# Performance work log

Hardware: AMD Instinct MI355X
Metric: run time of the kernel (lower is better)

The kernel has to match this reference:

```python
import jax, jax.numpy as jnp
import numpy as np

B, S, H, E = 8, 4096, 1024, 8
TEMPERATURE = 1.0


def setup_inputs() -> dict:
    key = jax.random.key(0)
    ks = jax.random.split(key, 7)
    s_h = 1.0 / np.sqrt(H).astype(np.float32)
    s_h2 = 1.0 / np.sqrt(H // 2).astype(np.float32)
    return {
        "hidden_states": jax.random.normal(ks[0], (B, S, H), jnp.float32),
        # routing_network: Linear(H, H//2) -> ReLU -> Linear(H//2, E)
        "W1": jax.random.normal(ks[1], (H, H // 2), jnp.float32) * s_h,
        "b1": jnp.zeros((H // 2,), jnp.float32),
        "W2": jax.random.normal(ks[2], (H // 2, E), jnp.float32) * s_h2,
        "b2": jnp.zeros((E,), jnp.float32),
        # per-expert dense transform (fixed stand-in for torch.randn-per-call)
        "expert_W": jax.random.normal(ks[3], (E, H, H), jnp.float32) * s_h,
        "expert_b": jax.random.normal(ks[4], (E, H), jnp.float32),
    }


def reference(hidden_states, W1, b1, W2, b2, expert_W, expert_b):
    # Routing network -> logits [B, S, E]
    h = jax.nn.relu(jnp.einsum("bsh,hf->bsf", hidden_states, W1) + b1)
    logits = jnp.einsum("bsf,fe->bse", h, W2) + b2
    probs = jax.nn.softmax(logits / TEMPERATURE, axis=-1)
    # top-1 expert per token (scores are NOT applied to output in the original)
    sel = jnp.argmax(probs, axis=-1)  # [B, S] int
    out = jnp.zeros_like(hidden_states)
    for e in range(E):  # small fixed loop over experts
        mask = (sel == e)[..., None].astype(hidden_states.dtype)  # [B, S, 1]
        xe = hidden_states * mask
        ye = jnp.einsum("bsh,hd->bsd", xe, expert_W[e]) + expert_b[e]
        out = out + ye * mask
    return out
```

## Files before the change

kernel.cpp:

```cpp
#include <hip/hip_runtime.h>
#include <hip/hip_bf16.h>
#include <stdint.h>

#define NTOK 32768
#define HD 1024
#define FD 512
#define NEXP 8
#define TAU 0.05f
#define TAU2 4e-4f

typedef __attribute__((ext_vector_type(8))) short short8;
typedef __attribute__((ext_vector_type(4))) float f32x4;

__device__ __forceinline__ short f2bh(float f) {
  uint32_t u = __float_as_uint(f);
  return (short)((u + 0x7fffu + ((u >> 16) & 1u)) >> 16);
}
__device__ __forceinline__ float bh2f(short h) {
  return __uint_as_float(((uint32_t)(uint16_t)h) << 16);
}

__device__ __forceinline__ void gl16(void* lds, const void* g) {
  __builtin_amdgcn_global_load_lds(
      (const __attribute__((address_space(1))) void*)g,
      (__attribute__((address_space(3))) void*)lds, 16, 0, 0);
}

#define WAITBAR(N)                                              \
  do {                                                          \
    asm volatile("s_waitcnt vmcnt(" #N ")" ::: "memory");       \
    __builtin_amdgcn_s_barrier();                               \
    asm volatile("" ::: "memory");                              \
  } while (0)
#define BARO()                                                  \
  do {                                                          \
    asm volatile("" ::: "memory");                              \
    __builtin_amdgcn_s_barrier();                               \
    asm volatile("" ::: "memory");                              \
  } while (0)

__global__ __launch_bounds__(256) void k_convert(const float* __restrict__ x,
                                                 short* __restrict__ xbf) {
  size_t i = ((size_t)blockIdx.x * 256 + threadIdx.x) * 8;
  f32x4 v0 = *(const f32x4*)(x + i);
  f32x4 v1 = *(const f32x4*)(x + i + 4);
  short8 o;
#pragma unroll
  for (int q = 0; q < 4; ++q) { o[q] = f2bh(v0[q]); o[4 + q] = f2bh(v1[q]); }
  *(short8*)(xbf + i) = o;
}

__global__ __launch_bounds__(256) void k_transpose(
    const float* __restrict__ src, short* __restrict__ dst, int rows, int cols) {
  __shared__ float tile[32][33];
  size_t msz = (size_t)rows * cols;
  src += (size_t)blockIdx.z * msz;
  dst += (size_t)blockIdx.z * msz;
  int c0 = blockIdx.x * 32, r0 = blockIdx.y * 32;
  int tx = threadIdx.x & 31, ty = threadIdx.x >> 5;
#pragma unroll
  for (int i = 0; i < 32; i += 8)
    tile[ty + i][tx] = src[(size_t)(r0 + ty + i) * cols + c0 + tx];
  __syncthreads();
#pragma unroll
  for (int i = 0; i < 32; i += 8)
    dst[(size_t)(c0 + ty + i) * rows + r0 + tx] = f2bh(tile[tx][ty + i]);
}

__global__ __launch_bounds__(256) void k_transpose_split(
    const float* __restrict__ src, short* __restrict__ dstH,
    short* __restrict__ dstL, int rows, int cols) {
  __shared__ float tile[32][33];
  int c0 = blockIdx.x * 32, r0 = blockIdx.y * 32;
  int tx = threadIdx.x & 31, ty = threadIdx.x >> 5;
#pragma unroll
  for (int i = 0; i < 32; i += 8)
    tile[ty + i][tx] = src[(size_t)(r0 + ty + i) * cols + c0 + tx];
  __syncthreads();
#pragma unroll
  for (int i = 0; i < 32; i += 8) {
    float v = tile[tx][ty + i];
    short h = f2bh(v);
    size_t di = (size_t)(c0 + ty + i) * rows + r0 + tx;
    dstH[di] = h;
    dstL[di] = f2bh(v - bh2f(h));
  }
}

template <bool ABF>
__global__ __launch_bounds__(256) void k_gemm1(
    const short* __restrict__ xbf, const float* __restrict__ xf,
    const short* __restrict__ W1T, const float* __restrict__ b1,
    const float* __restrict__ W2, float* __restrict__ part) {
  __shared__ __align__(16) char smem[39168];

  const int tid = threadIdx.x;
  const int lane = tid & 63, wave = tid >> 6;
  const int wr = wave >> 1, wc = wave & 1;
  const int fr = lane & 15, fg = lane >> 4;
  const int bx = ((blockIdx.x & 7) << 5) | (blockIdx.x >> 3);
  const int m0 = bx * 128, n0 = blockIdx.y * 128;
  const int by = blockIdx.y;

  const int r0 = wave * 16 + (lane >> 2);
  const int lsw = (((lane & 3) ^ ((lane >> 3) & 3)) << 3);
  const short* b0p = W1T + (size_t)(n0 + r0) * HD + lsw;
  const short* b1p = W1T + (size_t)(n0 + r0 + 64) * HD + lsw;

  const short* a0p = nullptr; const short* a1p = nullptr;
  const float* aF = nullptr;
  int ar = 0, ah = 0, p0e = 0, p1e = 0;
  if constexpr (ABF) {
    a0p = xbf + (size_t)(m0 + r0) * HD + lsw;
    a1p = xbf + (size_t)(m0 + r0 + 64) * HD + lsw;
  } else {
    ar = tid >> 1; ah = tid & 1;
    aF = xf + (size_t)(m0 + ar) * HD + ah * 16;
    int s = (ar >> 1) & 3;
    p0e = ((2 * ah) ^ s) << 3;
    p1e = p0e ^ 8;
  }

  f32x4 acc[4][4];
#pragma unroll
  for (int i = 0; i < 4; ++i)
#pragma unroll
    for (int j = 0; j < 4; ++j) acc[i][j] = (f32x4){0.f, 0.f, 0.f, 0.f};

  auto STAGE = [&](int kt, int b) {
    const int k0 = kt * 32;
    gl16(smem + 16384 + b * 8192 + wave * 1024, b0p + k0);
    gl16(smem + 16384 + b * 8192 + 4096 + wave * 1024, b1p + k0);
    if constexpr (ABF) {
      gl16(smem + b * 8192 + wave * 1024, a0p + k0);
      gl16(smem + b * 8192 + 4096 + wave * 1024, a1p + k0);
    } else {
      f32x4 u0 = *(const f32x4*)(aF + k0);
      f32x4 u1 = *(const f32x4*)(aF + k0 + 4);
      f32x4 u2 = *(const f32x4*)(aF + k0 + 8);
      f32x4 u3 = *(const f32x4*)(aF + k0 + 12);
      short8 s0, s1;
#pragma unroll
      for (int q = 0; q < 4; ++q) {
        s0[q] = f2bh(u0[q]); s0[4 + q] = f2bh(u1[q]);
        s1[q] = f2bh(u2[q]); s1[4 + q] = f2bh(u3[q]);
      }
      short* As = (short*)(smem + b * 8192);
      *(short8*)(As + ar * 32 + p0e) = s0;
      *(short8*)(As + ar * 32 + p1e) = s1;
    }
  };
  const int csw = (fr >> 1) & 3;
  auto COMPUTE = [&](int b) {
    const short* As = (const short*)(smem + b * 8192);
    const short* Bs = (const short*)(smem + 16384 + b * 8192);
    short8 af[4], bf4[4];
#pragma unroll
    for (int i = 0; i < 4; ++i) {
      af[i]  = *(const short8*)(As + (wr * 64 + i * 16 + fr) * 32 + ((fg ^ csw) << 3));
      bf4[i] = *(const short8*)(Bs + (wc * 64 + i * 16 + fr) * 32 + ((fg ^ csw) << 3));
    }
#pragma unroll
    for (int i = 0; i < 4; ++i)
#pragma unroll
      for (int j = 0; j < 4; ++j)
        acc[i][j] = __builtin_amdgcn_mfma_f32_16x16x32_bf16(af[i], bf4[j], acc[i][j], 0, 0, 0);
  };

  STAGE(0, 0);
  if constexpr (ABF) WAITBAR(0); else __syncthreads();
#pragma unroll 1
  for (int kt = 0; kt < 32; kt += 2) {
    STAGE(kt + 1, 1);
    if constexpr (ABF) WAITBAR(4); else __syncthreads();
    COMPUTE(0);
    if constexpr (ABF) BARO(); else __syncthreads();
    if (kt + 2 < 32) {
      STAGE(kt + 2, 0);
      if constexpr (ABF) WAITBAR(4); else __syncthreads();
    } else {
      if constexpr (ABF) WAITBAR(0); else __syncthreads();
    }
    COMPUTE(1);
    if constexpr (ABF) BARO(); else __syncthreads();
  }

  short* hbf = (short*)smem;
  short* W2b = (short*)(smem + 34816);
  float b1j[4];
#pragma unroll
  for (int j = 0; j < 4; ++j) b1j[j] = b1[n0 + wc * 64 + j * 16 + fr];
  for (int q = tid; q < 2048; q += 256) {
    int col = q >> 7, k = q & 127;
    W2b[col * 136 + k] = (col < 8) ? f2bh(W2[(size_t)(n0 + k) * 8 + col]) : (short)0;
  }
#pragma unroll
  for (int i = 0; i < 4; ++i)
#pragma unroll
    for (int j = 0; j < 4; ++j) {
      int col = wc * 64 + j * 16 + fr;
#pragma unroll
      for (int q = 0; q < 4; ++q)
        hbf[(wr * 64 + i * 16 + fg * 4 + q) * 136 + col] =
            f2bh(fmaxf(acc[i][j][q] + b1j[j], 0.f));
    }
  __syncthreads();
#pragma unroll
  for (int rg = 0; rg < 2; ++rg) {
    int row16 = wave * 32 + rg * 16;
    f32x4 accl = (f32x4){0.f, 0.f, 0.f, 0.f};
#pragma unroll
    for (int kk = 0; kk < 4; ++kk) {
      short8 a = *(const short8*)(hbf + (row16 + fr) * 136 + kk * 32 + fg * 8);
      short8 b = *(const short8*)(W2b + fr * 136 + kk * 32 + fg * 8);
      accl = __builtin_amdgcn_mfma_f32_16x16x32_bf16(a, b, accl, 0, 0, 0);
    }
    if (fr < 8) {
      float* pp = part + (size_t)(m0 + row16 + fg * 4) * 32 + by * 8 + fr;
#pragma unroll
      for (int q = 0; q < 4; ++q) pp[(size_t)q * 32] = accl[q];
    }
  }
}

__global__ __launch_bounds__(256) void k_combine(
    const float* __restrict__ part, const float* __restrict__ b2,
    int* __restrict__ sel, int* __restrict__ flagged, int* __restrict__ nflag) {
  int t = blockIdx.x * 256 + threadIdx.x;
  const float* p = part + (size_t)t * 32;
  float lg[8];
#pragma unroll
  for (int e = 0; e < 8; ++e) lg[e] = p[e] + p[8 + e] + p[16 + e] + p[24 + e] + b2[e];
  int be = 0; float best = lg[0];
#pragma unroll
  for (int e = 1; e < 8; ++e) if (lg[e] > best) { best = lg[e]; be = e; }
  float second = -3.4e38f;
#pragma unroll
  for (int e = 0; e < 8; ++e) if (e != be && lg[e] > second) second = lg[e];
  sel[t] = be;
  if (best - second < TAU) {
    int ix = atomicAdd(nflag, 1);
    if (ix < NTOK) flagged[ix] = t;
  }
}

__global__ __launch_bounds__(256) void k_gemmR(
    const float* __restrict__ x, const short* __restrict__ W1hT,
    const short* __restrict__ W1lT, const float* __restrict__ b1,
    const float* __restrict__ W2, const int* __restrict__ flagged,
    const int* __restrict__ nflag, float* __restrict__ partR) {
  __shared__ __align__(16) char smem[37888];
  __shared__ int toks[128];
  short* Ah = (short*)smem;
  short* Al = (short*)(smem + 8192);

  int nf = *nflag; if (nf > NTOK) nf = NTOK;
  const int m0 = blockIdx.x * 128;
  if (m0 >= nf) return;
  const int tid = threadIdx.x;
  if (tid < 128) {
    int s = m0 + tid;
    toks[tid] = flagged[s < nf ? s : nf - 1];
  }
  __syncthreads();

  const int lane = tid & 63, wave = tid >> 6;
  const int wr = wave >> 1, wc = wave & 1;
  const int fr = lane & 15, fg = lane >> 4;
  const int n0 = blockIdx.y * 128;
  const int by = blockIdx.y;

  const int off0 = wave * 1024 + lane * 16;
  const int off1 = off0 + 4096;
  const int r0 = off0 >> 6, c0 = (off0 & 63) >> 1;
  const int r1 = off1 >> 6, c1 = (off1 & 63) >> 1;
  const short* bh0p = W1hT + (size_t)(n0 + r0) * HD + c0;
  const short* bh1p = W1hT + (size_t)(n0 + r1) * HD + c1;
  const short* bl0p = W1lT + (size_t)(n0 + r0) * HD + c0;
  const short* bl1p = W1lT + (size_t)(n0 + r1) * HD + c1;
  char* ldsBh0 = smem + 16384 + wave * 1024;
  char* ldsBh1 = smem + 16384 + wave * 1024 + 4096;
  char* ldsBl0 = smem + 24576 + wave * 1024;
  char* ldsBl1 = smem + 24576 + wave * 1024 + 4096;
  const int ar = tid >> 1, ah2 = tid & 1;
  const float* aF = x + (size_t)toks[ar] * HD + ah2 * 16;

  f32x4 acc[4][4];
#pragma unroll
  for (int i = 0; i < 4; ++i)
#pragma unroll
    for (int j = 0; j < 4; ++j) acc[i][j] = (f32x4){0.f, 0.f, 0.f, 0.f};

  for (int k0 = 0; k0 < HD; k0 += 32) {
    gl16(ldsBh0, bh0p + k0);
    gl16(ldsBh1, bh1p + k0);
    gl16(ldsBl0, bl0p + k0);
    gl16(ldsBl1, bl1p + k0);
    f32x4 u0 = *(const f32x4*)(aF + k0);
    f32x4 u1 = *(const f32x4*)(aF + k0 + 4);
    f32x4 u2 = *(const f32x4*)(aF + k0 + 8);
    f32x4 u3 = *(const f32x4*)(aF + k0 + 12);
    short8 sh0, sh1, sl0, sl1;
#pragma unroll
    for (int q = 0; q < 4; ++q) {
      { float f = u0[q]; short h = f2bh(f); sh0[q]     = h; sl0[q]     = f2bh(f - bh2f(h)); }
      { float f = u1[q]; short h = f2bh(f); sh0[4 + q] = h; sl0[4 + q] = f2bh(f - bh2f(h)); }
      { float f = u2[q]; short h = f2bh(f); sh1[q]     = h; sl1[q]     = f2bh(f - bh2f(h)); }
      { float f = u3[q]; short h = f2bh(f); sh1[4 + q] = h; sl1[4 + q] = f2bh(f - bh2f(h)); }
    }
    *(short8*)(Ah + ar * 32 + ah2 * 16)     = sh0;
    *(short8*)(Ah + ar * 32 + ah2 * 16 + 8) = sh1;
    *(short8*)(Al + ar * 32 + ah2 * 16)     = sl0;
    *(short8*)(Al + ar * 32 + ah2 * 16 + 8) = sl1;
    __syncthreads();
    short8 af[4], alf[4], bf[4], blf[4];
#pragma unroll
    for (int i = 0; i < 4; ++i) {
      int row = (wr * 64 + i * 16 + fr) * 32 + fg * 8;
      af[i]  = *(const short8*)(Ah + row);
      alf[i] = *(const short8*)(Al + row);
      int rowb = (wc * 64 + i * 16 + fr) * 32 + fg * 8;
      bf[i]  = *(const short8*)((short*)(smem + 16384) + rowb);
      blf[i] = *(const short8*)((short*)(smem + 24576) + rowb);
    }
#pragma unroll
    for (int i = 0; i < 4; ++i)
#pragma unroll
      for (int j = 0; j < 4; ++j) {
        acc[i][j] = __builtin_amdgcn_mfma_f32_16x16x32_bf16(af[i],  bf[j],  acc[i][j], 0, 0, 0);
        acc[i][j] = __builtin_amdgcn_mfma_f32_16x16x32_bf16(af[i],  blf[j], acc[i][j], 0, 0, 0);
        acc[i][j] = __builtin_amdgcn_mfma_f32_16x16x32_bf16(alf[i], bf[j],  acc[i][j], 0, 0, 0);
      }
    __syncthreads();
  }

  float* hl64 = (float*)smem;
  float* W2c  = (float*)(smem + 33024);
  *(f32x4*)(W2c + tid * 4) = *(const f32x4*)(W2 + (size_t)n0 * NEXP + tid * 4);
  float b1j[4];
#pragma unroll
  for (int j = 0; j < 4; ++j) b1j[j] = b1[n0 + wc * 64 + j * 16 + fr];

  for (int p = 0; p < 2; ++p) {
    if (wr == p) {
#pragma unroll
      for (int i = 0; i < 4; ++i)
#pragma unroll
        for (int j = 0; j < 4; ++j) {
          int col = wc * 64 + j * 16 + fr;
#pragma unroll
          for (int q = 0; q < 4; ++q)
            hl64[(i * 16 + fg * 4 + q) * 129 + col] = fmaxf(acc[i][j][q] + b1j[j], 0.f);
        }
    }
    __syncthreads();
    if (tid < 128) {
      int r2 = tid & 63, eh = tid >> 6;
      const float* hrow = hl64 + r2 * 129;
      const float* wcp = W2c + eh * 4;
      float s0 = 0.f, s1 = 0.f, s2 = 0.f, s3 = 0.f;
      for (int f = 0; f < 128; ++f) {
        float hv = hrow[f];
        s0 += hv * wcp[f * 8 + 0];
        s1 += hv * wcp[f * 8 + 1];
        s2 += hv * wcp[f * 8 + 2];
        s3 += hv * wcp[f * 8 + 3];
      }
      float* pp = partR + (size_t)(m0 + p * 64 + r2) * 32 + by * 8 + eh * 4;
      pp[0] = s0; pp[1] = s1; pp[2] = s2; pp[3] = s3;
    }
    __syncthreads();
  }
}

__global__ __launch_bounds__(256) void k_combineR(
    const float* __restrict__ partR, const float* __restrict__ b2,
    const int* __restrict__ flagged, const int* __restrict__ nflag,
    int* __restrict__ sel, int* __restrict__ flagged2, int* __restrict__ nflag2) {
  int nf = *nflag; if (nf > NTOK) nf = NTOK;
  int s = blockIdx.x * 256 + threadIdx.x;
  if (s >= nf) return;
  int t = flagged[s];
  const float* p = partR + (size_t)s * 32;
  float lg[8];
#pragma unroll
  for (int e = 0; e < 8; ++e) lg[e] = p[e] + p[8 + e] + p[16 + e] + p[24 + e] + b2[e];
  int be = 0; float best = lg[0];
#pragma unroll
  for (int e = 1; e < 8; ++e) if (lg[e] > best) { best = lg[e]; be = e; }
  float second = -3.4e38f;
#pragma unroll
  for (int e = 0; e < 8; ++e) if (e != be && lg[e] > second) second = lg[e];
  sel[t] = be;
  if (best - second < TAU2) {
    int ix = atomicAdd(nflag2, 1);
    if (ix < NTOK) flagged2[ix] = t;
  }
}

__global__ __launch_bounds__(256) void k_recomputeB(
    const float* __restrict__ x, const float* __restrict__ W1,
    const float* __restrict__ b1, const float* __restrict__ W2,
    const float* __restrict__ b2, const int* __restrict__ flagged2,
    const int* __restrict__ nflag2, int* __restrict__ sel) {
  __shared__ float xs[1024];
  __shared__ double hs[512];
  __shared__ double red[8][32];
  __shared__ double lgd[8];
  int nf = *nflag2; if (nf > NTOK) nf = NTOK;
  const int tid = threadIdx.x;
  for (int ti = blockIdx.x; ti < nf; ti += gridDim.x) {
    int t = flagged2[ti];
    __syncthreads();
    for (int q = tid; q < 1024; q += 256) xs[q] = x[(size_t)t * HD + q];
    __syncthreads();
    int f0 = tid * 2;
    double a0 = 0.0, a1 = 0.0;
    for (int h = 0; h < 1024; h += 4) {
      float2 w0 = *(const float2*)(W1 + (size_t)(h + 0) * FD + f0);
      float2 w1 = *(const float2*)(W1 + (size_t)(h + 1) * FD + f0);
      float2 w2 = *(const float2*)(W1 + (size_t)(h + 2) * FD + f0);
      float2 w3 = *(const float2*)(W1 + (size_t)(h + 3) * FD + f0);
      double x0 = (double)xs[h], x1 = (double)xs[h + 1];
      double x2 = (double)xs[h + 2], x3 = (double)xs[h + 3];
      a0 += x0 * (double)w0.x; a1 += x0 * (double)w0.y;
      a0 += x1 * (double)w1.x; a1 += x1 * (double)w1.y;
      a0 += x2 * (double)w2.x; a1 += x2 * (double)w2.y;
      a0 += x3 * (double)w3.x; a1 += x3 * (double)w3.y;
    }
    a0 += (double)b1[f0]; a1 += (double)b1[f0 + 1];
    hs[f0]     = a0 > 0.0 ? a0 : 0.0;
    hs[f0 + 1] = a1 > 0.0 ? a1 : 0.0;
    __syncthreads();
    {
      int e = tid >> 5, c = tid & 31;
      int fb = c * 16;
      double s = 0.0;
#pragma unroll
      for (int ff = 0; ff < 16; ++ff)
        s += hs[fb + ff] * (double)W2[(size_t)(fb + ff) * 8 + e];
      red[e][c] = s;
    }
    __syncthreads();
    if (tid < 8) {
      double s = 0.0;
#pragma unroll
      for (int c = 0; c < 32; ++c) s += red[tid][c];
      lgd[tid] = s + (double)b2[tid];
    }
    __syncthreads();
    if (tid == 0) {
      int be = 0; double best = lgd[0];
#pragma unroll
      for (int e = 1; e < 8; ++e) if (lgd[e] > best) { best = lgd[e]; be = e; }
      sel[t] = be;
    }
    __syncthreads();
  }
}

__global__ __launch_bounds__(256) void k_compact(
    const int* __restrict__ sel, int* __restrict__ cnt, int* __restrict__ list) {
  __shared__ int wcnt[4][8];
  __shared__ int woff[4][8];
  __shared__ int bbase[8];
  const int tid = threadIdx.x, lane = tid & 63, wave = tid >> 6;
  const int t = blockIdx.x * 256 + tid;
  const int e = sel[t];
  const unsigned long long ltmask = (1ull << lane) - 1ull;
  int rank = 0;
#pragma unroll
  for (int e2 = 0; e2 < 8; ++e2) {
    unsigned long long m = __ballot(e == e2);
    if (e2 == e) rank = __popcll(m & ltmask);
    if (lane == 0) wcnt[wave][e2] = __popcll(m);
  }
  __syncthreads();
  if (tid < 8) {
    int s0 = wcnt[0][tid], s1 = wcnt[1][tid], s2 = wcnt[2][tid], s3 = wcnt[3][tid];
    woff[0][tid] = 0; woff[1][tid] = s0; woff[2][tid] = s0 + s1; woff[3][tid] = s0 + s1 + s2;
    bbase[tid] = atomicAdd(&cnt[tid], s0 + s1 + s2 + s3);
  }
  __syncthreads();
  list[(size_t)e * NTOK + bbase[e] + woff[wave][e] + rank] = t;
}

__global__ void k_build_desc(const int* __restrict__ cnt, int* __restrict__ desc,
                             int* __restrict__ ntl) {
  if (threadIdx.x == 0 && blockIdx.x == 0) {
    int n = 0;
    for (int e = 0; e < 8; ++e) {
      int m = (cnt[e] + 127) >> 7;
      for (int i = 0; i < m; ++i) desc[n++] = (e << 16) | i;
    }
    *ntl = n;
  }
}

template <bool ABF>
__global__ __launch_bounds__(256) void k_gemm2(
    const short* __restrict__ xbf, const float* __restrict__ xf,
    const short* __restrict__ WexpT, const float* __restrict__ expert_b,
    const int* __restrict__ cnt, const int* __restrict__ list,
    const int* __restrict__ desc, const int* __restrict__ ntl,
    float* __restrict__ out) {
  __shared__ __align__(16) char smem[32768];
  __shared__ int toks[128];
  const int bx = (blockIdx.x % 8) * 33 + blockIdx.x / 8;
  if (bx >= *ntl) return;
  int dsc = desc[bx];
  int e = dsc >> 16, mt = dsc & 0xffff;
  int ce = cnt[e];
  int mb = mt * 128;
  int rows = ce - mb; if (rows > 128) rows = 128;

  const int tid = threadIdx.x;
  if (tid < 128) {
    int idx = mb + tid;
    toks[tid] = list[(size_t)e * NTOK + (idx < ce ? idx : ce - 1)];
  }
  __syncthreads();

  const int lane = tid & 63, wave = tid >> 6;
  const int wr = wave >> 1, wc = wave & 1;
  const int fr = lane & 15, fg = lane >> 4;
  const int n0 = blockIdx.y * 128;

  const int r0 = wave * 16 + (lane >> 2);
  const int lsw = (((lane & 3) ^ ((lane >> 3) & 3)) << 3);
  const size_t ebase = (size_t)e << 20;
  const short* b0p = WexpT + ebase + (size_t)(n0 + r0) * HD + lsw;
  const short* b1p = WexpT + ebase + (size_t)(n0 + r0 + 64) * HD + lsw;

  const short* a0p = nullptr; const short* a1p = nullptr;
  const float* aF = nullptr;
  int ar = 0, ah = 0, p0e = 0, p1e = 0;
  if constexpr (ABF) {
    a0p = xbf + (size_t)toks[r0] * HD + lsw;
    a1p = xbf + (size_t)toks[r0 + 64] * HD + lsw;
  } else {
    ar = tid >> 1; ah = tid & 1;
    aF = xf + (size_t)toks[ar] * HD + ah * 16;
    int s = (ar >> 1) & 3;
    p0e = ((2 * ah) ^ s) << 3;
    p1e = p0e ^ 8;
  }

  f32x4 acc[4][4];
#pragma unroll
  for (int i = 0; i < 4; ++i)
#pragma unroll
    for (int j = 0; j < 4; ++j) acc[i][j] = (f32x4){0.f, 0.f, 0.f, 0.f};

  auto STAGE = [&](int kt, int b) {
    const int k0 = kt * 32;
    gl16(smem + 16384 + b * 8192 + wave * 1024, b0p + k0);
    gl16(smem + 16384 + b * 8192 + 4096 + wave * 1024, b1p + k0);
    if constexpr (ABF) {
      gl16(smem + b * 8192 + wave * 1024, a0p + k0);
      gl16(smem + b * 8192 + 4096 + wave * 1024, a1p + k0);
    } else {
      f32x4 u0 = *(const f32x4*)(aF + k0);
      f32x4 u1 = *(const f32x4*)(aF + k0 + 4);
      f32x4 u2 = *(const f32x4*)(aF + k0 + 8);
      f32x4 u3 = *(const f32x4*)(aF + k0 + 12);
      short8 s0, s1;
#pragma unroll
      for (int q = 0; q < 4; ++q) {
        s0[q] = f2bh(u0[q]); s0[4 + q] = f2bh(u1[q]);
        s1[q] = f2bh(u2[q]); s1[4 + q] = f2bh(u3[q]);
      }
      short* As = (short*)(smem + b * 8192);
      *(short8*)(As + ar * 32 + p0e) = s0;
      *(short8*)(As + ar * 32 + p1e) = s1;
    }
  };
  const int csw = (fr >> 1) & 3;
  auto COMPUTE = [&](int b) {
    const short* As = (const short*)(smem + b * 8192);
    const short* Bs = (const short*)(smem + 16384 + b * 8192);
    short8 af[4], bf4[4];
#pragma unroll
    for (int i = 0; i < 4; ++i) {
      af[i]  = *(const short8*)(As + (wr * 64 + i * 16 + fr) * 32 + ((fg ^ csw) << 3));
      bf4[i] = *(const short8*)(Bs + (wc * 64 + i * 16 + fr) * 32 + ((fg ^ csw) << 3));
    }
#pragma unroll
    for (int i = 0; i < 4; ++i)
#pragma unroll
      for (int j = 0; j < 4; ++j)
        acc[i][j] = __builtin_amdgcn_mfma_f32_16x16x32_bf16(af[i], bf4[j], acc[i][j], 0, 0, 0);
  };

  STAGE(0, 0);
  if constexpr (ABF) WAITBAR(0); else __syncthreads();
#pragma unroll 1
  for (int kt = 0; kt < 32; kt += 2) {
    STAGE(kt + 1, 1);
    if constexpr (ABF) WAITBAR(4); else __syncthreads();
    COMPUTE(0);
    if constexpr (ABF) BARO(); else __syncthreads();
    if (kt + 2 < 32) {
      STAGE(kt + 2, 0);
      if constexpr (ABF) WAITBAR(4); else __syncthreads();
    } else {
      if constexpr (ABF) WAITBAR(0); else __syncthreads();
    }
    COMPUTE(1);
    if constexpr (ABF) BARO(); else __syncthreads();
  }

  float ebv[4];
#pragma unroll
  for (int j = 0; j < 4; ++j) ebv[j] = expert_b[e * HD + n0 + wc * 64 + j * 16 + fr];
#pragma unroll
  for (int i = 0; i < 4; ++i)
#pragma unroll
    for (int j = 0; j < 4; ++j) {
      int col = n0 + wc * 64 + j * 16 + fr;
#pragma unroll
      for (int q = 0; q < 4; ++q) {
        int rr = wr * 64 + i * 16 + fg * 4 + q;
        if (rr < rows) out[(size_t)toks[rr] * HD + col] = acc[i][j][q] + ebv[j];
      }
    }
}

extern "C" void kernel_launch(void* const* d_in, const int* in_sizes, int n_in,
                              void* d_out, int out_size, void* d_ws, size_t ws_size,
                              hipStream_t stream) {
  const float* x  = (const float*)d_in[0];
  const float* W1 = (const float*)d_in[1];
  const float* b1 = (const float*)d_in[2];
  const float* W2 = (const float*)d_in[3];
  const float* b2 = (const float*)d_in[4];
  const float* eW = (const float*)d_in[5];
  const float* eb = (const float*)d_in[6];
  float* out = (float*)d_out;
  char* ws = (char*)d_ws;

  const size_t XBF_BYTES = (size_t)NTOK * HD * 2;
  size_t need_rest = 16777216ull + 1048576 + 4194304 + 131072 * 3 + 1048576 + 4096;
  bool big = ws_size >= XBF_BYTES + need_rest;

  size_t off = 0;
  short* xbf = nullptr;
  if (big) { xbf = (short*)ws; off += XBF_BYTES; }
  short* WexpT  = (short*)(ws + off); off += 16777216;
  short* W1T    = (short*)(ws + off); off += 1048576;
  float* part   = (float*)(ws + off); off += 4194304;
  int* sel      = (int*)(ws + off); off += 131072;
  int* flagged  = (int*)(ws + off); off += 131072;
  int* flagged2 = (int*)(ws + off); off += 131072;
  int* list     = (int*)(ws + off); off += 1048576;
  int* cnt      = (int*)(ws + off); off += 32;
  int* nflag    = (int*)(ws + off); off += 4;
  int* ntl      = (int*)(ws + off); off += 4;
  int* nflag2   = (int*)(ws + off); off += 24;
  int* desc     = (int*)(ws + off); off += 1088;
  if (ws_size < off) return;

  short* W1lT = (short*)list;

  hipMemsetAsync(cnt, 0, 44, stream);

  dim3 b256(256);
  if (big) k_convert<<<dim3(16384), b256, 0, stream>>>(x, xbf);
  k_transpose_split<<<dim3(16, 32), b256, 0, stream>>>(W1, W1T, W1lT, 1024, 512);
  k_transpose<<<dim3(32, 32, 8), b256, 0, stream>>>(eW, WexpT, 1024, 1024);
  if (big)
    k_gemm1<true><<<dim3(256, 4), b256, 0, stream>>>(xbf, nullptr, W1T, b1, W2, part);
  else
    k_gemm1<false><<<dim3(256, 4), b256, 0, stream>>>(nullptr, x, W1T, b1, W2, part);
  k_combine<<<dim3(128), b256, 0, stream>>>(part, b2, sel, flagged, nflag);
  k_gemmR<<<dim3(256, 4), b256, 0, stream>>>(x, W1T, W1lT, b1, W2, flagged, nflag, part);
  k_combineR<<<dim3(128), b256, 0, stream>>>(part, b2, flagged, nflag, sel, flagged2, nflag2);
  k_recomputeB<<<dim3(128), b256, 0, stream>>>(x, W1, b1, W2, b2, flagged2, nflag2, sel);
  k_compact<<<dim3(128), b256, 0, stream>>>(sel, cnt, list);
  k_build_desc<<<dim3(1), dim3(64), 0, stream>>>(cnt, desc, ntl);
  if (big)
    k_gemm2<true><<<dim3(264, 8), b256, 0, stream>>>(xbf, nullptr, WexpT, eb, cnt, list, desc, ntl, out);
  else
    k_gemm2<false><<<dim3(264, 8), b256, 0, stream>>>(nullptr, x, WexpT, eb, cnt, list, desc, ntl, out);
}
```

Measured before the change: 362.0 us.

## Deepen async LDS pipeline to triple buffering in both GEMM kernels

Replaces the double-buffered global_load_lds prefetch in the bf16-input paths of both GEMM kernels with a three-stage ring. Two tiles stay in flight while the third is computed, and a single wait+barrier is used per k-step. The fp32 fallback path is reduced to a simple single-buffer load/sync/compute loop. Shared memory per block grows to 48KB, which may lower occupancy.

```diff
diff --git a/kernel.cpp b/kernel.cpp
--- a/kernel.cpp
+++ b/kernel.cpp
@@ -92,7 +92,7 @@
     const short* __restrict__ xbf, const float* __restrict__ xf,
     const short* __restrict__ W1T, const float* __restrict__ b1,
     const float* __restrict__ W2, float* __restrict__ part) {
-  __shared__ __align__(16) char smem[39168];
+  __shared__ __align__(16) char smem[49152];
 
   const int tid = threadIdx.x;
   const int lane = tid & 63, wave = tid >> 6;
@@ -127,14 +127,44 @@
 #pragma unroll
     for (int j = 0; j < 4; ++j) acc[i][j] = (f32x4){0.f, 0.f, 0.f, 0.f};
 
-  auto STAGE = [&](int kt, int b) {
-    const int k0 = kt * 32;
-    gl16(smem + 16384 + b * 8192 + wave * 1024, b0p + k0);
-    gl16(smem + 16384 + b * 8192 + 4096 + wave * 1024, b1p + k0);
-    if constexpr (ABF) {
+  const int csw = (fr >> 1) & 3;
+  auto COMPUTE = [&](int b) {
+    const short* As = (const short*)(smem + b * 8192);
+    const short* Bs = (const short*)(smem + 24576 + b * 8192);
+    short8 af[4], bf4[4];
+#pragma unroll
+    for (int i = 0; i < 4; ++i) {
+      af[i]  = *(const short8*)(As + (wr * 64 + i * 16 + fr) * 32 + ((fg ^ csw) << 3));
+      bf4[i] = *(const short8*)(Bs + (wc * 64 + i * 16 + fr) * 32 + ((fg ^ csw) << 3));
+    }
+#pragma unroll
+    for (int i = 0; i < 4; ++i)
+#pragma unroll
+      for (int j = 0; j < 4; ++j)
+        acc[i][j] = __builtin_amdgcn_mfma_f32_16x16x32_bf16(af[i], bf4[j], acc[i][j], 0, 0, 0);
+  };
+
+  if constexpr (ABF) {
+    auto STAGE = [&](int kt, int b) {
+      const int k0 = kt * 32;
+      gl16(smem + 24576 + b * 8192 + wave * 1024, b0p + k0);
+      gl16(smem + 24576 + b * 8192 + 4096 + wave * 1024, b1p + k0);
       gl16(smem + b * 8192 + wave * 1024, a0p + k0);
       gl16(smem + b * 8192 + 4096 + wave * 1024, a1p + k0);
-    } else {
+    };
+    STAGE(0, 0); STAGE(1, 1); STAGE(2, 2);
+#pragma unroll 1
+    for (int t = 0; t < 32; ++t) {
+      if (t < 30) WAITBAR(8); else if (t == 30) WAITBAR(4); else WAITBAR(0);
+      COMPUTE(t % 3);
+      BARO();
+      if (t < 29) STAGE(t + 3, t % 3);
+    }
+  } else {
+    auto STAGEF = [&](int kt) {
+      const int k0 = kt * 32;
+      gl16(smem + 24576 + wave * 1024, b0p + k0);
+      gl16(smem + 24576 + 4096 + wave * 1024, b1p + k0);
       f32x4 u0 = *(const f32x4*)(aF + k0);
       f32x4 u1 = *(const f32x4*)(aF + k0 + 4);
       f32x4 u2 = *(const f32x4*)(aF + k0 + 8);
@@ -145,44 +175,17 @@
         s0[q] = f2bh(u0[q]); s0[4 + q] = f2bh(u1[q]);
         s1[q] = f2bh(u2[q]); s1[4 + q] = f2bh(u3[q]);
       }
-      short* As = (short*)(smem + b * 8192);
+      short* As = (short*)smem;
       *(short8*)(As + ar * 32 + p0e) = s0;
       *(short8*)(As + ar * 32 + p1e) = s1;
-    }
-  };
-  const int csw = (fr >> 1) & 3;
-  auto COMPUTE = [&](int b) {
-    const short* As = (const short*)(smem + b * 8192);
-    const short* Bs = (const short*)(smem + 16384 + b * 8192);
-    short8 af[4], bf4[4];
-#pragma unroll
-    for (int i = 0; i < 4; ++i) {
-      af[i]  = *(const short8*)(As + (wr * 64 + i * 16 + fr) * 32 + ((fg ^ csw) << 3));
-      bf4[i] = *(const short8*)(Bs + (wc * 64 + i * 16 + fr) * 32 + ((fg ^ csw) << 3));
-    }
-#pragma unroll
-    for (int i = 0; i < 4; ++i)
-#pragma unroll
-      for (int j = 0; j < 4; ++j)
-        acc[i][j] = __builtin_amdgcn_mfma_f32_16x16x32_bf16(af[i], bf4[j], acc[i][j], 0, 0, 0);
-  };
-
-  STAGE(0, 0);
-  if constexpr (ABF) WAITBAR(0); else __syncthreads();
+    };
 #pragma unroll 1
-  for (int kt = 0; kt < 32; kt += 2) {
-    STAGE(kt + 1, 1);
-    if constexpr (ABF) WAITBAR(4); else __syncthreads();
-    COMPUTE(0);
-    if constexpr (ABF) BARO(); else __syncthreads();
-    if (kt + 2 < 32) {
-      STAGE(kt + 2, 0);
-      if constexpr (ABF) WAITBAR(4); else __syncthreads();
-    } else {
-      if constexpr (ABF) WAITBAR(0); else __syncthreads();
-    }
-    COMPUTE(1);
-    if constexpr (ABF) BARO(); else __syncthreads();
+    for (int kt = 0; kt < 32; ++kt) {
+      STAGEF(kt);
+      __syncthreads();
+      COMPUTE(0);
+      __syncthreads();
+    }
   }
 
   short* hbf = (short*)smem;
@@ -504,7 +507,7 @@
     const int* __restrict__ cnt, const int* __restrict__ list,
     const int* __restrict__ desc, const int* __restrict__ ntl,
     float* __restrict__ out) {
-  __shared__ __align__(16) char smem[32768];
+  __shared__ __align__(16) char smem[49152];
   __shared__ int toks[128];
   const int bx = (blockIdx.x % 8) * 33 + blockIdx.x / 8;
   if (bx >= *ntl) return;
@@ -552,14 +555,44 @@
 #pragma unroll
     for (int j = 0; j < 4; ++j) acc[i][j] = (f32x4){0.f, 0.f, 0.f, 0.f};
 
-  auto STAGE = [&](int kt, int b) {
-    const int k0 = kt * 32;
-    gl16(smem + 16384 + b * 8192 + wave * 1024, b0p + k0);
-    gl16(smem + 16384 + b * 8192 + 4096 + wave * 1024, b1p + k0);
-    if constexpr (ABF) {
+  const int csw = (fr >> 1) & 3;
+  auto COMPUTE = [&](int b) {
+    const short* As = (const short*)(smem + b * 8192);
+    const short* Bs = (const short*)(smem + 24576 + b * 8192);
+    short8 af[4], bf4[4];
+#pragma unroll
+    for (int i = 0; i < 4; ++i) {
+      af[i]  = *(const short8*)(As + (wr * 64 + i * 16 + fr) * 32 + ((fg ^ csw) << 3));
+      bf4[i] = *(const short8*)(Bs + (wc * 64 + i * 16 + fr) * 32 + ((fg ^ csw) << 3));
+    }
+#pragma unroll
+    for (int i = 0; i < 4; ++i)
+#pragma unroll
+      for (int j = 0; j < 4; ++j)
+        acc[i][j] = __builtin_amdgcn_mfma_f32_16x16x32_bf16(af[i], bf4[j], acc[i][j], 0, 0, 0);
+  };
+
+  if constexpr (ABF) {
+    auto STAGE = [&](int kt, int b) {
+      const int k0 = kt * 32;
+      gl16(smem + 24576 + b * 8192 + wave * 1024, b0p + k0);
+      gl16(smem + 24576 + b * 8192 + 4096 + wave * 1024, b1p + k0);
       gl16(smem + b * 8192 + wave * 1024, a0p + k0);
       gl16(smem + b * 8192 + 4096 + wave * 1024, a1p + k0);
-    } else {
+    };
+    STAGE(0, 0); STAGE(1, 1); STAGE(2, 2);
+#pragma unroll 1
+    for (int t = 0; t < 32; ++t) {
+      if (t < 30) WAITBAR(8); else if (t == 30) WAITBAR(4); else WAITBAR(0);
+      COMPUTE(t % 3);
+      BARO();
+      if (t < 29) STAGE(t + 3, t % 3);
+    }
+  } else {
+    auto STAGEF = [&](int kt) {
+      const int k0 = kt * 32;
+      gl16(smem + 24576 + wave * 1024, b0p + k0);
+      gl16(smem + 24576 + 4096 + wave * 1024, b1p + k0);
       f32x4 u0 = *(const f32x4*)(aF + k0);
       f32x4 u1 = *(const f32x4*)(aF + k0 + 4);
       f32x4 u2 = *(const f32x4*)(aF + k0 + 8);
@@ -570,44 +603,17 @@
         s0[q] = f2bh(u0[q]); s0[4 + q] = f2bh(u1[q]);
         s1[q] = f2bh(u2[q]); s1[4 + q] = f2bh(u3[q]);
       }
-      short* As = (short*)(smem + b * 8192);
+      short* As = (short*)smem;
       *(short8*)(As + ar * 32 + p0e) = s0;
       *(short8*)(As + ar * 32 + p1e) = s1;
-    }
-  };
-  const int csw = (fr >> 1) & 3;
-  auto COMPUTE = [&](int b) {
-    const short* As = (const short*)(smem + b * 8192);
-    const short* Bs = (const short*)(smem + 16384 + b * 8192);
-    short8 af[4], bf4[4];
-#pragma unroll
-    for (int i = 0; i < 4; ++i) {
-      af[i]  = *(const short8*)(As + (wr * 64 + i * 16 + fr) * 32 + ((fg ^ csw) << 3));
-      bf4[i] = *(const short8*)(Bs + (wc * 64 + i * 16 + fr) * 32 + ((fg ^ csw) << 3));
-    }
-#pragma unroll
-    for (int i = 0; i < 4; ++i)
-#pragma unroll
-      for (int j = 0; j < 4; ++j)
-        acc[i][j] = __builtin_amdgcn_mfma_f32_16x16x32_bf16(af[i], bf4[j], acc[i][j], 0, 0, 0);
-  };
-
-  STAGE(0, 0);
-  if constexpr (ABF) WAITBAR(0); else __syncthreads();
+    };
 #pragma unroll 1
-  for (int kt = 0; kt < 32; kt += 2) {
-    STAGE(kt + 1, 1);
-    if constexpr (ABF) WAITBAR(4); else __syncthreads();
-    COMPUTE(0);
-    if constexpr (ABF) BARO(); else __syncthreads();
-    if (kt + 2 < 32) {
-      STAGE(kt + 2, 0);
-      if constexpr (ABF) WAITBAR(4); else __syncthreads();
-    } else {
-      if constexpr (ABF) WAITBAR(0); else __syncthreads();
-    }
-    COMPUTE(1);
-    if constexpr (ABF) BARO(); else __syncthreads();
+    for (int kt = 0; kt < 32; ++kt) {
+      STAGEF(kt);
+      __syncthreads();
+      COMPUTE(0);
+      __syncthreads();
+    }
   }
 
   float ebv[4];
```

After: 352.8 us. 2.5% less time.
